# Optimization experiments

Hardware: AMD Instinct MI355X
Metric: run time of the kernel (lower is better)

Reference implementation:

```python
import jax
import jax.numpy as jnp
import numpy as np

NC = 80
TOPK = 10
STRIDES = (8, 16, 32)
GRIDS = ((80, 80), (40, 40), (20, 20))
ALPHA = 1.0
BETA = 6.0
EPS = 1e-9
B = 32
G = 20


def _pairwise_iou(b1, b2):
    # b1: [A,4], b2: [G,4] in x1y1x2y2 -> [A,G]
    lt = jnp.maximum(b1[:, None, :2], b2[None, :, :2])
    rb = jnp.minimum(b1[:, None, 2:], b2[None, :, 2:])
    wh = jnp.clip(rb - lt, 0.0)
    inter = wh[..., 0] * wh[..., 1]
    a1 = (b1[:, 2] - b1[:, 0]) * (b1[:, 3] - b1[:, 1])
    a2 = (b2[:, 2] - b2[:, 0]) * (b2[:, 3] - b2[:, 1])
    return inter / (a1[:, None] + a2[None, :] - inter + EPS)


def _assign_one(scores, reg, anchors, labels, boxes, stride):
    # Task-aligned assignment for one image at one FPN level.
    # scores: [A,NC] softmax probs, reg: [A,4] ltrb in stride units,
    # anchors: [A,2] grid centers, labels: [G] int, boxes: [G,4] pixels.
    A = scores.shape[0]
    g = labels.shape[0]
    anc_pix = anchors * stride                                    # [A,2]
    pd_boxes = jnp.concatenate(
        [anc_pix - reg[:, :2] * stride, anc_pix + reg[:, 2:] * stride], axis=-1
    )                                                             # [A,4]
    iou = _pairwise_iou(pd_boxes, boxes)                          # [A,G]
    cls_score = scores[:, labels]                                 # [A,G]
    align = (cls_score ** ALPHA) * (iou ** BETA)                  # [A,G]
    # candidate anchors: center strictly inside gt box
    lt_ok = (anc_pix[:, None, :] - boxes[None, :, :2]) > EPS
    rb_ok = (boxes[None, :, 2:] - anc_pix[:, None, :]) > EPS
    in_gts = jnp.all(jnp.concatenate([lt_ok, rb_ok], axis=-1), axis=-1)  # [A,G]
    metric = jnp.where(in_gts, align, 0.0)
    # top-k anchors per gt by alignment metric
    vals, idx = jax.lax.top_k(metric.T, TOPK)                     # [G,K]
    topk_mask = jnp.zeros((g, A), bool).at[jnp.arange(g)[:, None], idx].set(vals > EPS)
    is_pos = topk_mask.T & in_gts                                 # [A,G]
    # resolve anchors assigned to multiple gts by max IoU
    n_assign = is_pos.sum(axis=-1)
    best_gt = jnp.argmax(jnp.where(is_pos, iou, -1.0), axis=-1)   # [A]
    best_oh = jax.nn.one_hot(best_gt, g, dtype=bool)
    is_pos = jnp.where((n_assign > 1)[:, None], best_oh & is_pos, is_pos)
    fg_mask = is_pos.any(axis=-1)                                 # [A]
    assigned = jnp.argmax(is_pos, axis=-1)                        # [A]
    target_labels = jnp.where(fg_mask, labels[assigned], 0)
    return target_labels, fg_mask


def _level_loss(cls, reg, anc, gt_labels, gt_boxes, stride):
    # cls: [B,A,NC] logits, reg: [B,A,4], anc: [A,2]
    scores = jax.nn.softmax(jax.lax.stop_gradient(cls), axis=-1)
    tl, fg = jax.vmap(
        lambda s, r, l, b: _assign_one(s, r, anc, l, b, stride)
    )(scores, jax.lax.stop_gradient(reg), gt_labels, gt_boxes)
    logp = jax.nn.log_softmax(cls, axis=-1)
    ce = -jnp.take_along_axis(logp, tl[..., None], axis=-1)[..., 0]  # [B,A]
    return (ce * fg.astype(cls.dtype)).sum(), fg.sum()


def setup_inputs() -> dict:
    key = jax.random.key(0)
    ks = jax.random.split(key, 10)
    inp = {}
    for i, (h, w) in enumerate(GRIDS):
        inp[f"pred_cls_{i}"] = jax.random.normal(ks[i], (B, h * w, NC), jnp.float32)
        inp[f"pred_reg_{i}"] = jax.random.uniform(ks[3 + i], (B, h * w, 4), jnp.float32) * 4.0
    ancs = []
    for (h, w) in GRIDS:
        yy, xx = jnp.meshgrid(
            jnp.arange(h, dtype=jnp.float32) + 0.5,
            jnp.arange(w, dtype=jnp.float32) + 0.5,
            indexing="ij",
        )
        ancs.append(jnp.stack([xx.ravel(), yy.ravel()], axis=-1))
    inp["anchor_points"] = jnp.concatenate(ancs, axis=0)  # [8400,2] grid units
    cxcy = jax.random.uniform(ks[6], (B, G, 2), jnp.float32) * 600.0 + 20.0
    wh = jax.random.uniform(ks[7], (B, G, 2), jnp.float32) * 120.0 + 16.0
    boxes = jnp.concatenate([cxcy - wh / 2, cxcy + wh / 2], axis=-1)
    inp["gt_boxes"] = jnp.clip(boxes, 0.0, 640.0)
    inp["gt_labels"] = jax.random.randint(ks[8], (B, G), 0, NC)
    return inp


def reference(pred_cls_0, pred_cls_1, pred_cls_2,
              pred_reg_0, pred_reg_1, pred_reg_2,
              anchor_points, gt_boxes, gt_labels):
    pred_cls = [pred_cls_0, pred_cls_1, pred_cls_2]
    pred_reg = [pred_reg_0, pred_reg_1, pred_reg_2]
    sizes = [c.shape[1] for c in pred_cls]
    offs = np.cumsum([0] + sizes)
    total = jnp.zeros((), jnp.float32)
    n_pos = jnp.zeros((), jnp.int32)
    for i in range(3):
        anc = anchor_points[offs[i]:offs[i + 1]]
        l, k = _level_loss(pred_cls[i], pred_reg[i], anc, gt_labels, gt_boxes, STRIDES[i])
        total = total + l
        n_pos = n_pos + k.astype(jnp.int32)
    loss = total / jnp.maximum(n_pos, 1).astype(jnp.float32)
    return loss, n_pos
```

## Files before the change

### kernel.cpp

```cpp
#include <hip/hip_runtime.h>
#include <cstdint>
#include <cstddef>

#define NCLS 80
#define KTOP 10
#define NG   20
#define NB   32
#define A0   6400
#define A1   1600
#define A2   400
#define ATOT 8400
#define EPSF 1e-9f

#define NTHR   (NB * ATOT)
#define NBLK   ((NTHR + 255) / 256)
#define RECTCAP 512

__global__ __launch_bounds__(256) void phase1_logz(
    const float* __restrict__ cls0, const float* __restrict__ cls1,
    const float* __restrict__ cls2,
    const float* __restrict__ anchors, const float* __restrict__ gtb,
    float* __restrict__ logZ, uint32_t* __restrict__ mask)
{
    int t = blockIdx.x * 256 + threadIdx.x;
    if (t >= NTHR) return;
    mask[t] = 0;
    int b = t / ATOT, a = t % ATOT;

    const float* cls; int A; float stride;
    if (a < A0)           { cls = cls0; A = A0; stride = 8.f;  }
    else if (a < A0 + A1) { cls = cls1; A = A1; stride = 16.f; }
    else                  { cls = cls2; A = A2; stride = 32.f; }
    int al = (a < A0) ? a : (a < A0 + A1 ? a - A0 : a - A0 - A1);

    float ax = anchors[2 * a]     * stride;
    float ay = anchors[2 * a + 1] * stride;

    const float4* gb4 = reinterpret_cast<const float4*>(gtb + (size_t)b * NG * 4);
    bool any = false;
    #pragma unroll
    for (int g = 0; g < NG; ++g) {
        float4 gv = gb4[g];
        any = any || ((ax - gv.x > EPSF) && (ay - gv.y > EPSF) &&
                      (gv.z - ax > EPSF) && (gv.w - ay > EPSF));
    }
    if (!any) return;

    const float4* crow4 = reinterpret_cast<const float4*>(cls + ((size_t)b * A + al) * NCLS);
    float r[NCLS];
    float m = -1e30f;
    #pragma unroll
    for (int j = 0; j < NCLS / 4; ++j) {
        float4 v = crow4[j];
        r[4*j+0] = v.x; r[4*j+1] = v.y; r[4*j+2] = v.z; r[4*j+3] = v.w;
        m = fmaxf(m, fmaxf(fmaxf(v.x, v.y), fmaxf(v.z, v.w)));
    }
    float s = 0.f;
    #pragma unroll
    for (int c = 0; c < NCLS; ++c) s += __expf(r[c] - m);
    logZ[(size_t)b * ATOT + a] = m + __logf(s);
}

__global__ __launch_bounds__(64) void phase2_topk(
    const float* __restrict__ cls0, const float* __restrict__ reg0,
    const float* __restrict__ cls1, const float* __restrict__ reg1,
    const float* __restrict__ cls2, const float* __restrict__ reg2,
    const float* __restrict__ gtb, const int* __restrict__ gtl,
    const float* __restrict__ logZ, uint32_t* __restrict__ mask)
{
    int id  = blockIdx.x;
    int lvl = id % 3;
    int bg  = id / 3;
    int b = bg / NG, g = bg % NG;
    int lane = threadIdx.x;

    const float* cls; const float* reg; int off, A, W; float stride;
    if (lvl == 0)      { cls = cls0; reg = reg0; off = 0;     A = A0; W = 80; stride = 8.f;  }
    else if (lvl == 1) { cls = cls1; reg = reg1; off = A0;    A = A1; W = 40; stride = 16.f; }
    else               { cls = cls2; reg = reg2; off = A0+A1; A = A2; W = 20; stride = 32.f; }

    float4 gv = reinterpret_cast<const float4*>(gtb + (size_t)b * NG * 4)[g];
    int lbl = gtl[b * NG + g];

    float inv = 1.f / stride;
    int ix0 = max(0,     (int)floorf(gv.x * inv - 0.5f));
    int ix1 = min(W - 1, (int)ceilf (gv.z * inv - 0.5f));
    int iy0 = max(0,     (int)floorf(gv.y * inv - 0.5f));
    int iy1 = min(W - 1, (int)ceilf (gv.w * inv - 0.5f));
    int nx = ix1 - ix0 + 1, ny = iy1 - iy0 + 1;
    if (nx <= 0 || ny <= 0) return;
    int n = nx * ny; if (n > RECTCAP) n = RECTCAP;

    float area2 = (gv.z - gv.x) * (gv.w - gv.y);

    __shared__ unsigned long long key[RECTCAP];
    for (int i = lane; i < n; i += 64) {
        int iy = i / nx, ix = i - iy * nx;
        int gx = ix0 + ix, gy = iy0 + iy;
        float ax = ((float)gx + 0.5f) * stride;
        float ay = ((float)gy + 0.5f) * stride;
        unsigned long long kk = 0;
        bool ing = (ax - gv.x > EPSF) && (ay - gv.y > EPSF) &&
                   (gv.z - ax > EPSF) && (gv.w - ay > EPSF);
        if (ing) {
            int al = gy * W + gx;
            int a  = off + al;
            float4 rr = *reinterpret_cast<const float4*>(reg + ((size_t)b * A + al) * 4);
            float px1 = ax - rr.x * stride, py1 = ay - rr.y * stride;
            float px2 = ax + rr.z * stride, py2 = ay + rr.w * stride;
            float area1 = (px2 - px1) * (py2 - py1);
            float ltx = fmaxf(px1, gv.x), lty = fmaxf(py1, gv.y);
            float rbx = fminf(px2, gv.z), rby = fminf(py2, gv.w);
            float w = fmaxf(rbx - ltx, 0.f), h = fmaxf(rby - lty, 0.f);
            float inter = w * h;
            float iou = inter / (area1 + area2 - inter + EPSF);
            float lz = logZ[(size_t)b * ATOT + a];
            float c  = cls[((size_t)b * A + al) * NCLS + lbl];
            float sc = __expf(c - lz);
            float i2 = iou * iou;
            float met = sc * (i2 * i2 * i2);
            if (met > EPSF)
                kk = ((unsigned long long)__float_as_uint(met) << 32)
                   | (uint32_t)(ATOT - a);
        }
        key[i] = kk;
    }
    __syncthreads();

    for (int k = 0; k < KTOP; ++k) {
        unsigned long long bk = 0; int bs = -1;
        for (int i = lane; i < n; i += 64) {
            unsigned long long kk = key[i];
            if (kk > bk) { bk = kk; bs = i; }
        }
        #pragma unroll
        for (int sft = 32; sft > 0; sft >>= 1) {
            unsigned long long ok = __shfl_down(bk, sft);
            int os = __shfl_down(bs, sft);
            if (ok > bk) { bk = ok; bs = os; }
        }
        bk = __shfl(bk, 0); bs = __shfl(bs, 0);
        if (bk == 0) break;
        if (lane == 0) {
            int aa = ATOT - (int)(bk & 0xffffffffu);
            atomicOr(&mask[(size_t)b * ATOT + aa], 1u << g);
            key[bs] = 0;
        }
        __syncthreads();
    }
}

__global__ __launch_bounds__(256) void phase3_loss(
    const float* __restrict__ cls0, const float* __restrict__ reg0,
    const float* __restrict__ cls1, const float* __restrict__ reg1,
    const float* __restrict__ cls2, const float* __restrict__ reg2,
    const float* __restrict__ anchors, const float* __restrict__ gtb,
    const int* __restrict__ gtl,
    const uint32_t* __restrict__ mask, const float* __restrict__ logZ,
    float2* __restrict__ partials)
{
    int t = blockIdx.x * 256 + threadIdx.x;
    float ce = 0.f; float pc = 0.f;

    if (t < NTHR) {
        int b = t / ATOT, a = t % ATOT;
        uint32_t mk = mask[(size_t)b * ATOT + a];
        if (mk) {
            const float* cls; const float* reg; int off, A; float stride;
            if (a < A0)           { cls = cls0; reg = reg0; off = 0;     A = A0; stride = 8.f;  }
            else if (a < A0 + A1) { cls = cls1; reg = reg1; off = A0;    A = A1; stride = 16.f; }
            else                  { cls = cls2; reg = reg2; off = A0+A1; A = A2; stride = 32.f; }
            int al = a - off;

            float ax = anchors[2 * a]     * stride;
            float ay = anchors[2 * a + 1] * stride;
            float4 rr = *reinterpret_cast<const float4*>(reg + ((size_t)b * A + al) * 4);
            float px1 = ax - rr.x * stride, py1 = ay - rr.y * stride;
            float px2 = ax + rr.z * stride, py2 = ay + rr.w * stride;
            float area1 = (px2 - px1) * (py2 - py1);

            const float4* gb4 = reinterpret_cast<const float4*>(gtb + (size_t)b * NG * 4);

            float bestI = -1.f; int bestG = 0;
            uint32_t mm = mk;
            while (mm) {
                int g = __ffs(mm) - 1; mm &= mm - 1;
                float4 gv = gb4[g];
                float ltx = fmaxf(px1, gv.x), lty = fmaxf(py1, gv.y);
                float rbx = fminf(px2, gv.z), rby = fminf(py2, gv.w);
                float w = fmaxf(rbx - ltx, 0.f), h = fmaxf(rby - lty, 0.f);
                float inter = w * h;
                float area2 = (gv.z - gv.x) * (gv.w - gv.y);
                float iou = inter / (area1 + area2 - inter + EPSF);
                if (iou > bestI) { bestI = iou; bestG = g; }
            }
            int tl = gtl[b * NG + bestG];
            const float* crow = cls + ((size_t)b * A + al) * NCLS;
            ce = logZ[(size_t)b * ATOT + a] - crow[tl];
            pc = 1.f;
        }
    }

    #pragma unroll
    for (int sft = 32; sft > 0; sft >>= 1) {
        ce += __shfl_down(ce, sft);
        pc += __shfl_down(pc, sft);
    }
    __shared__ float sce[4];
    __shared__ float spc[4];
    int wid = threadIdx.x >> 6, lane = threadIdx.x & 63;
    if (lane == 0) { sce[wid] = ce; spc[wid] = pc; }
    __syncthreads();
    if (threadIdx.x == 0) {
        float2 p;
        p.x = sce[0] + sce[1] + sce[2] + sce[3];
        p.y = spc[0] + spc[1] + spc[2] + spc[3];
        partials[blockIdx.x] = p;
    }
}

__global__ __launch_bounds__(256) void finalize_loss(
    const float2* __restrict__ partials, float* __restrict__ out)
{
    float ce = 0.f, pc = 0.f;
    for (int i = threadIdx.x; i < NBLK; i += 256) {
        float2 p = partials[i];
        ce += p.x; pc += p.y;
    }
    #pragma unroll
    for (int sft = 32; sft > 0; sft >>= 1) {
        ce += __shfl_down(ce, sft);
        pc += __shfl_down(pc, sft);
    }
    __shared__ float sce[4];
    __shared__ float spc[4];
    int wid = threadIdx.x >> 6, lane = threadIdx.x & 63;
    if (lane == 0) { sce[wid] = ce; spc[wid] = pc; }
    __syncthreads();
    if (threadIdx.x == 0) {
        float total = sce[0] + sce[1] + sce[2] + sce[3];
        int   n     = (int)(spc[0] + spc[1] + spc[2] + spc[3]);
        float denom = (float)(n < 1 ? 1 : n);
        out[0] = total / denom;
        out[1] = (float)n;
    }
}

extern "C" void kernel_launch(void* const* d_in, const int* in_sizes, int n_in,
                              void* d_out, int out_size, void* d_ws, size_t ws_size,
                              hipStream_t stream)
{
    const float* cls0 = (const float*)d_in[0];
    const float* reg0 = (const float*)d_in[1];
    const float* cls1 = (const float*)d_in[2];
    const float* reg1 = (const float*)d_in[3];
    const float* cls2 = (const float*)d_in[4];
    const float* reg2 = (const float*)d_in[5];
    const float* anchors = (const float*)d_in[6];
    const float* gtb  = (const float*)d_in[7];
    const int*   gtl  = (const int*)d_in[8];

    float*    logZ     = (float*)d_ws;
    uint32_t* mask     = (uint32_t*)(logZ + (size_t)NB * ATOT);
    float2*   partials = (float2*)(mask + (size_t)NB * ATOT);

    phase1_logz<<<NBLK, 256, 0, stream>>>(cls0, cls1, cls2, anchors, gtb, logZ, mask);
    phase2_topk<<<NB * NG * 3, 64, 0, stream>>>(cls0, reg0, cls1, reg1, cls2, reg2,
                                                gtb, gtl, logZ, mask);
    phase3_loss<<<NBLK, 256, 0, stream>>>(cls0, reg0, cls1, reg1, cls2, reg2,
                                          anchors, gtb, gtl, mask, logZ, partials);
    finalize_loss<<<1, 256, 0, stream>>>(partials, (float*)d_out);
}
```

Before: 36.77 us.

## Replace dense anchor passes with sparse top-k winner lists and per-gt conflict resolution

Removes the dense per-anchor logZ pass and the dense mask/loss pass. Each (image, gt, level) block now computes log-softmax only for candidate anchors inside its gt rectangle, then writes its top-k winners with their IoU to a compact list. A second kernel resolves anchors claimed by several gts by scanning the winner lists of all gts at the same level, then computes cross-entropy only for the anchors it keeps. This cuts memory traffic and launches, but the logsumexp is now recomputed redundantly for anchors that fall inside several gt rectangles.

```diff
diff --git a/kernel.cpp b/kernel.cpp
--- a/kernel.cpp
+++ b/kernel.cpp
@@ -11,62 +11,14 @@
 #define A2   400
 #define ATOT 8400
 #define EPSF 1e-9f
-
-#define NTHR   (NB * ATOT)
-#define NBLK   ((NTHR + 255) / 256)
 #define RECTCAP 512
 
-__global__ __launch_bounds__(256) void phase1_logz(
-    const float* __restrict__ cls0, const float* __restrict__ cls1,
-    const float* __restrict__ cls2,
-    const float* __restrict__ anchors, const float* __restrict__ gtb,
-    float* __restrict__ logZ, uint32_t* __restrict__ mask)
-{
-    int t = blockIdx.x * 256 + threadIdx.x;
-    if (t >= NTHR) return;
-    mask[t] = 0;
-    int b = t / ATOT, a = t % ATOT;
-
-    const float* cls; int A; float stride;
-    if (a < A0)           { cls = cls0; A = A0; stride = 8.f;  }
-    else if (a < A0 + A1) { cls = cls1; A = A1; stride = 16.f; }
-    else                  { cls = cls2; A = A2; stride = 32.f; }
-    int al = (a < A0) ? a : (a < A0 + A1 ? a - A0 : a - A0 - A1);
-
-    float ax = anchors[2 * a]     * stride;
-    float ay = anchors[2 * a + 1] * stride;
-
-    const float4* gb4 = reinterpret_cast<const float4*>(gtb + (size_t)b * NG * 4);
-    bool any = false;
-    #pragma unroll
-    for (int g = 0; g < NG; ++g) {
-        float4 gv = gb4[g];
-        any = any || ((ax - gv.x > EPSF) && (ay - gv.y > EPSF) &&
-                      (gv.z - ax > EPSF) && (gv.w - ay > EPSF));
-    }
-    if (!any) return;
-
-    const float4* crow4 = reinterpret_cast<const float4*>(cls + ((size_t)b * A + al) * NCLS);
-    float r[NCLS];
-    float m = -1e30f;
-    #pragma unroll
-    for (int j = 0; j < NCLS / 4; ++j) {
-        float4 v = crow4[j];
-        r[4*j+0] = v.x; r[4*j+1] = v.y; r[4*j+2] = v.z; r[4*j+3] = v.w;
-        m = fmaxf(m, fmaxf(fmaxf(v.x, v.y), fmaxf(v.z, v.w)));
-    }
-    float s = 0.f;
-    #pragma unroll
-    for (int c = 0; c < NCLS; ++c) s += __expf(r[c] - m);
-    logZ[(size_t)b * ATOT + a] = m + __logf(s);
-}
-
-__global__ __launch_bounds__(64) void phase2_topk(
+__global__ __launch_bounds__(64) void k1_topk(
     const float* __restrict__ cls0, const float* __restrict__ reg0,
     const float* __restrict__ cls1, const float* __restrict__ reg1,
     const float* __restrict__ cls2, const float* __restrict__ reg2,
     const float* __restrict__ gtb, const int* __restrict__ gtl,
-    const float* __restrict__ logZ, uint32_t* __restrict__ mask)
+    int2* __restrict__ winners)
 {
     int id  = blockIdx.x;
     int lvl = id % 3;
@@ -88,18 +40,20 @@
     int iy0 = max(0,     (int)floorf(gv.y * inv - 0.5f));
     int iy1 = min(W - 1, (int)ceilf (gv.w * inv - 0.5f));
     int nx = ix1 - ix0 + 1, ny = iy1 - iy0 + 1;
-    if (nx <= 0 || ny <= 0) return;
-    int n = nx * ny; if (n > RECTCAP) n = RECTCAP;
+    int n = (nx > 0 && ny > 0) ? nx * ny : 0;
+    if (n > RECTCAP) n = RECTCAP;
 
     float area2 = (gv.z - gv.x) * (gv.w - gv.y);
 
     __shared__ unsigned long long key[RECTCAP];
+    __shared__ float iouA[RECTCAP];
+
     for (int i = lane; i < n; i += 64) {
         int iy = i / nx, ix = i - iy * nx;
         int gx = ix0 + ix, gy = iy0 + iy;
         float ax = ((float)gx + 0.5f) * stride;
         float ay = ((float)gy + 0.5f) * stride;
-        unsigned long long kk = 0;
+        unsigned long long kk = 0; float iou = 0.f;
         bool ing = (ax - gv.x > EPSF) && (ay - gv.y > EPSF) &&
                    (gv.z - ax > EPSF) && (gv.w - ay > EPSF);
         if (ing) {
@@ -113,17 +67,32 @@
             float rbx = fminf(px2, gv.z), rby = fminf(py2, gv.w);
             float w = fmaxf(rbx - ltx, 0.f), h = fmaxf(rby - lty, 0.f);
             float inter = w * h;
-            float iou = inter / (area1 + area2 - inter + EPSF);
-            float lz = logZ[(size_t)b * ATOT + a];
-            float c  = cls[((size_t)b * A + al) * NCLS + lbl];
-            float sc = __expf(c - lz);
+            iou = inter / (area1 + area2 - inter + EPSF);
+
+            const float4* crow4 =
+                reinterpret_cast<const float4*>(cls + ((size_t)b * A + al) * NCLS);
+            float r[NCLS];
+            float m = -1e30f;
+            #pragma unroll
+            for (int j = 0; j < NCLS / 4; ++j) {
+                float4 v = crow4[j];
+                r[4*j+0] = v.x; r[4*j+1] = v.y; r[4*j+2] = v.z; r[4*j+3] = v.w;
+                m = fmaxf(m, fmaxf(fmaxf(v.x, v.y), fmaxf(v.z, v.w)));
+            }
+            float s = 0.f;
+            #pragma unroll
+            for (int c = 0; c < NCLS; ++c) s += __expf(r[c] - m);
+            float lz = m + __logf(s);
+
+            float cl = cls[((size_t)b * A + al) * NCLS + lbl];
+            float sc = __expf(cl - lz);
             float i2 = iou * iou;
             float met = sc * (i2 * i2 * i2);
             if (met > EPSF)
                 kk = ((unsigned long long)__float_as_uint(met) << 32)
                    | (uint32_t)(ATOT - a);
         }
-        key[i] = kk;
+        key[i] = kk; iouA[i] = iou;
     }
     __syncthreads();
 
@@ -140,64 +109,76 @@
             if (ok > bk) { bk = ok; bs = os; }
         }
         bk = __shfl(bk, 0); bs = __shfl(bs, 0);
-        if (bk == 0) break;
+        if (bk == 0) {
+            if (lane >= k && lane < KTOP)
+                winners[(size_t)id * KTOP + lane] = make_int2(-1, 0);
+            break;
+        }
         if (lane == 0) {
             int aa = ATOT - (int)(bk & 0xffffffffu);
-            atomicOr(&mask[(size_t)b * ATOT + aa], 1u << g);
+            winners[(size_t)id * KTOP + k] = make_int2(aa, __float_as_int(iouA[bs]));
             key[bs] = 0;
         }
         __syncthreads();
     }
 }
 
-__global__ __launch_bounds__(256) void phase3_loss(
-    const float* __restrict__ cls0, const float* __restrict__ reg0,
-    const float* __restrict__ cls1, const float* __restrict__ reg1,
-    const float* __restrict__ cls2, const float* __restrict__ reg2,
-    const float* __restrict__ anchors, const float* __restrict__ gtb,
-    const int* __restrict__ gtl,
-    const uint32_t* __restrict__ mask, const float* __restrict__ logZ,
-    float2* __restrict__ partials)
-{
-    int t = blockIdx.x * 256 + threadIdx.x;
-    float ce = 0.f; float pc = 0.f;
-
-    if (t < NTHR) {
-        int b = t / ATOT, a = t % ATOT;
-        uint32_t mk = mask[(size_t)b * ATOT + a];
-        if (mk) {
-            const float* cls; const float* reg; int off, A; float stride;
-            if (a < A0)           { cls = cls0; reg = reg0; off = 0;     A = A0; stride = 8.f;  }
-            else if (a < A0 + A1) { cls = cls1; reg = reg1; off = A0;    A = A1; stride = 16.f; }
-            else                  { cls = cls2; reg = reg2; off = A0+A1; A = A2; stride = 32.f; }
-            int al = a - off;
-
-            float ax = anchors[2 * a]     * stride;
-            float ay = anchors[2 * a + 1] * stride;
-            float4 rr = *reinterpret_cast<const float4*>(reg + ((size_t)b * A + al) * 4);
-            float px1 = ax - rr.x * stride, py1 = ay - rr.y * stride;
-            float px2 = ax + rr.z * stride, py2 = ay + rr.w * stride;
-            float area1 = (px2 - px1) * (py2 - py1);
-
-            const float4* gb4 = reinterpret_cast<const float4*>(gtb + (size_t)b * NG * 4);
-
-            float bestI = -1.f; int bestG = 0;
-            uint32_t mm = mk;
-            while (mm) {
-                int g = __ffs(mm) - 1; mm &= mm - 1;
-                float4 gv = gb4[g];
-                float ltx = fmaxf(px1, gv.x), lty = fmaxf(py1, gv.y);
-                float rbx = fminf(px2, gv.z), rby = fminf(py2, gv.w);
-                float w = fmaxf(rbx - ltx, 0.f), h = fmaxf(rby - lty, 0.f);
-                float inter = w * h;
-                float area2 = (gv.z - gv.x) * (gv.w - gv.y);
-                float iou = inter / (area1 + area2 - inter + EPSF);
-                if (iou > bestI) { bestI = iou; bestG = g; }
+__global__ __launch_bounds__(64) void k2_resolve(
+    const float* __restrict__ cls0, const float* __restrict__ cls1,
+    const float* __restrict__ cls2, const int* __restrict__ gtl,
+    const int2* __restrict__ winners, float2* __restrict__ partials)
+{
+    int id = blockIdx.x;
+    int b = id / NG, g = id % NG;
+    int lane = threadIdx.x;
+
+    __shared__ int2 sh[NG * 3 * KTOP];
+    for (int i = lane; i < NG * 3 * KTOP; i += 64)
+        sh[i] = winners[(size_t)b * NG * 3 * KTOP + i];
+    __syncthreads();
+
+    float ce = 0.f, pc = 0.f;
+    if (lane < 3 * KTOP) {
+        int2 e = sh[g * 3 * KTOP + lane];
+        if (e.x >= 0) {
+            float eiou = __int_as_float(e.y);
+            int lvl_e = lane / KTOP;
+            bool beaten = false;
+            for (int gf = 0; gf < NG; ++gf) {
+                #pragma unroll
+                for (int s = 0; s < KTOP; ++s) {
+                    int2 f = sh[(gf * 3 + lvl_e) * KTOP + s];
+                    if (f.x == e.x) {
+                        float fiou = __int_as_float(f.y);
+                        if (fiou > eiou || (fiou == eiou && gf < g)) beaten = true;
+                    }
+                }
             }
-            int tl = gtl[b * NG + bestG];
-            const float* crow = cls + ((size_t)b * A + al) * NCLS;
-            ce = logZ[(size_t)b * ATOT + a] - crow[tl];
-            pc = 1.f;
+            if (!beaten) {
+                int a = e.x;
+                const float* cls; int A, off;
+                if (a < A0)           { cls = cls0; A = A0; off = 0;     }
+                else if (a < A0 + A1) { cls = cls1; A = A1; off = A0;    }
+                else                  { cls = cls2; A = A2; off = A0+A1; }
+                int al = a - off;
+                const float4* crow4 =
+                    reinterpret_cast<const float4*>(cls + ((size_t)b * A + al) * NCLS);
+                float r[NCLS];
+                float m = -1e30f;
+                #pragma unroll
+                for (int j = 0; j < NCLS / 4; ++j) {
+                    float4 v = crow4[j];
+                    r[4*j+0] = v.x; r[4*j+1] = v.y; r[4*j+2] = v.z; r[4*j+3] = v.w;
+                    m = fmaxf(m, fmaxf(fmaxf(v.x, v.y), fmaxf(v.z, v.w)));
+                }
+                float s2 = 0.f;
+                #pragma unroll
+                for (int c = 0; c < NCLS; ++c) s2 += __expf(r[c] - m);
+                float lz = m + __logf(s2);
+                int tl = gtl[b * NG + g];
+                ce = lz - cls[((size_t)b * A + al) * NCLS + tl];
+                pc = 1.f;
+            }
         }
     }
 
@@ -206,24 +187,14 @@
         ce += __shfl_down(ce, sft);
         pc += __shfl_down(pc, sft);
     }
-    __shared__ float sce[4];
-    __shared__ float spc[4];
-    int wid = threadIdx.x >> 6, lane = threadIdx.x & 63;
-    if (lane == 0) { sce[wid] = ce; spc[wid] = pc; }
-    __syncthreads();
-    if (threadIdx.x == 0) {
-        float2 p;
-        p.x = sce[0] + sce[1] + sce[2] + sce[3];
-        p.y = spc[0] + spc[1] + spc[2] + spc[3];
-        partials[blockIdx.x] = p;
-    }
-}
-
-__global__ __launch_bounds__(256) void finalize_loss(
+    if (lane == 0) partials[id] = make_float2(ce, pc);
+}
+
+__global__ __launch_bounds__(256) void k3_finalize(
     const float2* __restrict__ partials, float* __restrict__ out)
 {
     float ce = 0.f, pc = 0.f;
-    for (int i = threadIdx.x; i < NBLK; i += 256) {
+    for (int i = threadIdx.x; i < NB * NG; i += 256) {
         float2 p = partials[i];
         ce += p.x; pc += p.y;
     }
@@ -256,18 +227,14 @@
     const float* reg1 = (const float*)d_in[3];
     const float* cls2 = (const float*)d_in[4];
     const float* reg2 = (const float*)d_in[5];
-    const float* anchors = (const float*)d_in[6];
     const float* gtb  = (const float*)d_in[7];
     const int*   gtl  = (const int*)d_in[8];
 
-    float*    logZ     = (float*)d_ws;
-    uint32_t* mask     = (uint32_t*)(logZ + (size_t)NB * ATOT);
-    float2*   partials = (float2*)(mask + (size_t)NB * ATOT);
-
-    phase1_logz<<<NBLK, 256, 0, stream>>>(cls0, cls1, cls2, anchors, gtb, logZ, mask);
-    phase2_topk<<<NB * NG * 3, 64, 0, stream>>>(cls0, reg0, cls1, reg1, cls2, reg2,
-                                                gtb, gtl, logZ, mask);
-    phase3_loss<<<NBLK, 256, 0, stream>>>(cls0, reg0, cls1, reg1, cls2, reg2,
-                                          anchors, gtb, gtl, mask, logZ, partials);
-    finalize_loss<<<1, 256, 0, stream>>>(partials, (float*)d_out);
-}
+    int2*   winners  = (int2*)d_ws;
+    float2* partials = (float2*)(winners + NB * NG * 3 * KTOP);
+
+    k1_topk<<<NB * NG * 3, 64, 0, stream>>>(cls0, reg0, cls1, reg1, cls2, reg2,
+                                            gtb, gtl, winners);
+    k2_resolve<<<NB * NG, 64, 0, stream>>>(cls0, cls1, cls2, gtl, winners, partials);
+    k3_finalize<<<1, 256, 0, stream>>>(partials, (float*)d_out);
+}
```

Result: slower. 44.40 us (median of 3 runs) (+20.7%).

## Fuse top-k selection and conflict resolution into one per-image-level kernel

Applied to the files above, without the earlier changes.

Replaces the per-(image,gt,level) top-k kernel, the global mask array, and the full-grid loss pass with a single kernel per (image,level). Each wave handles five gts, keeps candidate keys in registers, and records winners with their IoU in shared memory. Anchors claimed by several gts are resolved by scanning that shared list, which removes the mask writes, the atomics and one full-size launch. The cost is fewer, heavier blocks (96) with serial per-wave work and a rectangle cap of 512 candidates per gt.

```diff
diff --git a/kernel.cpp b/kernel.cpp
--- a/kernel.cpp
+++ b/kernel.cpp
@@ -14,17 +14,16 @@
 
 #define NTHR   (NB * ATOT)
 #define NBLK   ((NTHR + 255) / 256)
-#define RECTCAP 512
-
-__global__ __launch_bounds__(256) void phase1_logz(
+#define KREG   8
+
+__global__ __launch_bounds__(256) void k1_logz(
     const float* __restrict__ cls0, const float* __restrict__ cls1,
     const float* __restrict__ cls2,
     const float* __restrict__ anchors, const float* __restrict__ gtb,
-    float* __restrict__ logZ, uint32_t* __restrict__ mask)
+    float* __restrict__ logZ)
 {
     int t = blockIdx.x * 256 + threadIdx.x;
     if (t >= NTHR) return;
-    mask[t] = 0;
     int b = t / ATOT, a = t % ATOT;
 
     const float* cls; int A; float stride;
@@ -61,143 +60,128 @@
     logZ[(size_t)b * ATOT + a] = m + __logf(s);
 }
 
-__global__ __launch_bounds__(64) void phase2_topk(
+__global__ __launch_bounds__(256) void k2_select_resolve(
     const float* __restrict__ cls0, const float* __restrict__ reg0,
     const float* __restrict__ cls1, const float* __restrict__ reg1,
     const float* __restrict__ cls2, const float* __restrict__ reg2,
     const float* __restrict__ gtb, const int* __restrict__ gtl,
-    const float* __restrict__ logZ, uint32_t* __restrict__ mask)
+    const float* __restrict__ logZ, float2* __restrict__ partials)
 {
     int id  = blockIdx.x;
     int lvl = id % 3;
-    int bg  = id / 3;
-    int b = bg / NG, g = bg % NG;
-    int lane = threadIdx.x;
+    int b   = id / 3;
+    int tid = threadIdx.x, wave = tid >> 6, lane = tid & 63;
 
     const float* cls; const float* reg; int off, A, W; float stride;
     if (lvl == 0)      { cls = cls0; reg = reg0; off = 0;     A = A0; W = 80; stride = 8.f;  }
     else if (lvl == 1) { cls = cls1; reg = reg1; off = A0;    A = A1; W = 40; stride = 16.f; }
     else               { cls = cls2; reg = reg2; off = A0+A1; A = A2; W = 20; stride = 32.f; }
 
-    float4 gv = reinterpret_cast<const float4*>(gtb + (size_t)b * NG * 4)[g];
-    int lbl = gtl[b * NG + g];
-
+    __shared__ int2 win[NG * KTOP];
+    for (int i = tid; i < NG * KTOP; i += 256) win[i] = make_int2(-1, 0);
+    __syncthreads();
+
+    const float4* gb4 = reinterpret_cast<const float4*>(gtb + (size_t)b * NG * 4);
     float inv = 1.f / stride;
-    int ix0 = max(0,     (int)floorf(gv.x * inv - 0.5f));
-    int ix1 = min(W - 1, (int)ceilf (gv.z * inv - 0.5f));
-    int iy0 = max(0,     (int)floorf(gv.y * inv - 0.5f));
-    int iy1 = min(W - 1, (int)ceilf (gv.w * inv - 0.5f));
-    int nx = ix1 - ix0 + 1, ny = iy1 - iy0 + 1;
-    if (nx <= 0 || ny <= 0) return;
-    int n = nx * ny; if (n > RECTCAP) n = RECTCAP;
-
-    float area2 = (gv.z - gv.x) * (gv.w - gv.y);
-
-    __shared__ unsigned long long key[RECTCAP];
-    for (int i = lane; i < n; i += 64) {
-        int iy = i / nx, ix = i - iy * nx;
-        int gx = ix0 + ix, gy = iy0 + iy;
-        float ax = ((float)gx + 0.5f) * stride;
-        float ay = ((float)gy + 0.5f) * stride;
-        unsigned long long kk = 0;
-        bool ing = (ax - gv.x > EPSF) && (ay - gv.y > EPSF) &&
-                   (gv.z - ax > EPSF) && (gv.w - ay > EPSF);
-        if (ing) {
-            int al = gy * W + gx;
-            int a  = off + al;
-            float4 rr = *reinterpret_cast<const float4*>(reg + ((size_t)b * A + al) * 4);
-            float px1 = ax - rr.x * stride, py1 = ay - rr.y * stride;
-            float px2 = ax + rr.z * stride, py2 = ay + rr.w * stride;
-            float area1 = (px2 - px1) * (py2 - py1);
-            float ltx = fmaxf(px1, gv.x), lty = fmaxf(py1, gv.y);
-            float rbx = fminf(px2, gv.z), rby = fminf(py2, gv.w);
-            float w = fmaxf(rbx - ltx, 0.f), h = fmaxf(rby - lty, 0.f);
-            float inter = w * h;
-            float iou = inter / (area1 + area2 - inter + EPSF);
-            float lz = logZ[(size_t)b * ATOT + a];
-            float c  = cls[((size_t)b * A + al) * NCLS + lbl];
-            float sc = __expf(c - lz);
-            float i2 = iou * iou;
-            float met = sc * (i2 * i2 * i2);
-            if (met > EPSF)
-                kk = ((unsigned long long)__float_as_uint(met) << 32)
-                   | (uint32_t)(ATOT - a);
+
+    for (int gg = 0; gg < 5; ++gg) {
+        int g = wave * 5 + gg;
+        float4 gv = gb4[g];
+        int lbl = gtl[b * NG + g];
+
+        int ix0 = max(0,     (int)floorf(gv.x * inv - 0.5f));
+        int ix1 = min(W - 1, (int)ceilf (gv.z * inv - 0.5f));
+        int iy0 = max(0,     (int)floorf(gv.y * inv - 0.5f));
+        int iy1 = min(W - 1, (int)ceilf (gv.w * inv - 0.5f));
+        int nx = ix1 - ix0 + 1, ny = iy1 - iy0 + 1;
+        int n = (nx > 0 && ny > 0) ? nx * ny : 0;
+        if (n > KREG * 64) n = KREG * 64;
+
+        float area2 = (gv.z - gv.x) * (gv.w - gv.y);
+
+        unsigned long long kreg[KREG]; float ioureg[KREG];
+        #pragma unroll
+        for (int j = 0; j < KREG; ++j) {
+            kreg[j] = 0; ioureg[j] = 0.f;
+            int i = j * 64 + lane;
+            if (i < n) {
+                int iy = i / nx, ix = i - iy * nx;
+                int gx = ix0 + ix, gy = iy0 + iy;
+                float ax = ((float)gx + 0.5f) * stride;
+                float ay = ((float)gy + 0.5f) * stride;
+                bool ing = (ax - gv.x > EPSF) && (ay - gv.y > EPSF) &&
+                           (gv.z - ax > EPSF) && (gv.w - ay > EPSF);
+                if (ing) {
+                    int al = gy * W + gx;
+                    int a  = off + al;
+                    float4 rr = *reinterpret_cast<const float4*>(reg + ((size_t)b * A + al) * 4);
+                    float px1 = ax - rr.x * stride, py1 = ay - rr.y * stride;
+                    float px2 = ax + rr.z * stride, py2 = ay + rr.w * stride;
+                    float area1 = (px2 - px1) * (py2 - py1);
+                    float ltx = fmaxf(px1, gv.x), lty = fmaxf(py1, gv.y);
+                    float rbx = fminf(px2, gv.z), rby = fminf(py2, gv.w);
+                    float w = fmaxf(rbx - ltx, 0.f), h = fmaxf(rby - lty, 0.f);
+                    float inter = w * h;
+                    float iou = inter / (area1 + area2 - inter + EPSF);
+                    float lz = logZ[(size_t)b * ATOT + a];
+                    float c  = cls[((size_t)b * A + al) * NCLS + lbl];
+                    float sc = __expf(c - lz);
+                    float i2 = iou * iou;
+                    float met = sc * (i2 * i2 * i2);
+                    if (met > EPSF) {
+                        kreg[j] = ((unsigned long long)__float_as_uint(met) << 32)
+                                | (uint32_t)(ATOT - a);
+                        ioureg[j] = iou;
+                    }
+                }
+            }
         }
-        key[i] = kk;
-    }
-    __syncthreads();
-
-    for (int k = 0; k < KTOP; ++k) {
-        unsigned long long bk = 0; int bs = -1;
-        for (int i = lane; i < n; i += 64) {
-            unsigned long long kk = key[i];
-            if (kk > bk) { bk = kk; bs = i; }
+
+        for (int k = 0; k < KTOP; ++k) {
+            unsigned long long bk = 0;
+            #pragma unroll
+            for (int j = 0; j < KREG; ++j) if (kreg[j] > bk) bk = kreg[j];
+            #pragma unroll
+            for (int sft = 32; sft > 0; sft >>= 1) {
+                unsigned long long ok = __shfl_down(bk, sft);
+                if (ok > bk) bk = ok;
+            }
+            bk = __shfl(bk, 0);
+            if (bk == 0) break;
+            #pragma unroll
+            for (int j = 0; j < KREG; ++j) {
+                if (kreg[j] == bk) {
+                    int aa = ATOT - (int)(bk & 0xffffffffu);
+                    win[g * KTOP + k] = make_int2(aa, __float_as_int(ioureg[j]));
+                    kreg[j] = 0;
+                }
+            }
         }
-        #pragma unroll
-        for (int sft = 32; sft > 0; sft >>= 1) {
-            unsigned long long ok = __shfl_down(bk, sft);
-            int os = __shfl_down(bs, sft);
-            if (ok > bk) { bk = ok; bs = os; }
-        }
-        bk = __shfl(bk, 0); bs = __shfl(bs, 0);
-        if (bk == 0) break;
-        if (lane == 0) {
-            int aa = ATOT - (int)(bk & 0xffffffffu);
-            atomicOr(&mask[(size_t)b * ATOT + aa], 1u << g);
-            key[bs] = 0;
-        }
-        __syncthreads();
-    }
-}
-
-__global__ __launch_bounds__(256) void phase3_loss(
-    const float* __restrict__ cls0, const float* __restrict__ reg0,
-    const float* __restrict__ cls1, const float* __restrict__ reg1,
-    const float* __restrict__ cls2, const float* __restrict__ reg2,
-    const float* __restrict__ anchors, const float* __restrict__ gtb,
-    const int* __restrict__ gtl,
-    const uint32_t* __restrict__ mask, const float* __restrict__ logZ,
-    float2* __restrict__ partials)
-{
-    int t = blockIdx.x * 256 + threadIdx.x;
-    float ce = 0.f; float pc = 0.f;
-
-    if (t < NTHR) {
-        int b = t / ATOT, a = t % ATOT;
-        uint32_t mk = mask[(size_t)b * ATOT + a];
-        if (mk) {
-            const float* cls; const float* reg; int off, A; float stride;
-            if (a < A0)           { cls = cls0; reg = reg0; off = 0;     A = A0; stride = 8.f;  }
-            else if (a < A0 + A1) { cls = cls1; reg = reg1; off = A0;    A = A1; stride = 16.f; }
-            else                  { cls = cls2; reg = reg2; off = A0+A1; A = A2; stride = 32.f; }
-            int al = a - off;
-
-            float ax = anchors[2 * a]     * stride;
-            float ay = anchors[2 * a + 1] * stride;
-            float4 rr = *reinterpret_cast<const float4*>(reg + ((size_t)b * A + al) * 4);
-            float px1 = ax - rr.x * stride, py1 = ay - rr.y * stride;
-            float px2 = ax + rr.z * stride, py2 = ay + rr.w * stride;
-            float area1 = (px2 - px1) * (py2 - py1);
-
-            const float4* gb4 = reinterpret_cast<const float4*>(gtb + (size_t)b * NG * 4);
-
-            float bestI = -1.f; int bestG = 0;
-            uint32_t mm = mk;
-            while (mm) {
-                int g = __ffs(mm) - 1; mm &= mm - 1;
-                float4 gv = gb4[g];
-                float ltx = fmaxf(px1, gv.x), lty = fmaxf(py1, gv.y);
-                float rbx = fminf(px2, gv.z), rby = fminf(py2, gv.w);
-                float w = fmaxf(rbx - ltx, 0.f), h = fmaxf(rby - lty, 0.f);
-                float inter = w * h;
-                float area2 = (gv.z - gv.x) * (gv.w - gv.y);
-                float iou = inter / (area1 + area2 - inter + EPSF);
-                if (iou > bestI) { bestI = iou; bestG = g; }
-            }
-            int tl = gtl[b * NG + bestG];
-            const float* crow = cls + ((size_t)b * A + al) * NCLS;
-            ce = logZ[(size_t)b * ATOT + a] - crow[tl];
-            pc = 1.f;
+    }
+    __syncthreads();
+
+    float ce = 0.f, pc = 0.f;
+    if (tid < NG * KTOP) {
+        int2 e = win[tid];
+        if (e.x >= 0) {
+            int g = tid / KTOP;
+            float eiou = __int_as_float(e.y);
+            bool beaten = false;
+            for (int i = 0; i < NG * KTOP; ++i) {
+                int2 f = win[i];
+                if (f.x == e.x) {
+                    float fiou = __int_as_float(f.y);
+                    int gf = i / KTOP;
+                    if (fiou > eiou || (fiou == eiou && gf < g)) beaten = true;
+                }
+            }
+            if (!beaten) {
+                int a = e.x, al = a - off;
+                float lz = logZ[(size_t)b * ATOT + a];
+                int tl = gtl[b * NG + g];
+                ce = lz - cls[((size_t)b * A + al) * NCLS + tl];
+                pc = 1.f;
+            }
         }
     }
 
@@ -208,38 +192,37 @@
     }
     __shared__ float sce[4];
     __shared__ float spc[4];
-    int wid = threadIdx.x >> 6, lane = threadIdx.x & 63;
-    if (lane == 0) { sce[wid] = ce; spc[wid] = pc; }
-    __syncthreads();
-    if (threadIdx.x == 0) {
+    if (lane == 0) { sce[wave] = ce; spc[wave] = pc; }
+    __syncthreads();
+    if (tid == 0) {
         float2 p;
         p.x = sce[0] + sce[1] + sce[2] + sce[3];
         p.y = spc[0] + spc[1] + spc[2] + spc[3];
-        partials[blockIdx.x] = p;
-    }
-}
-
-__global__ __launch_bounds__(256) void finalize_loss(
+        partials[id] = p;
+    }
+}
+
+__global__ __launch_bounds__(128) void k3_finalize(
     const float2* __restrict__ partials, float* __restrict__ out)
 {
     float ce = 0.f, pc = 0.f;
-    for (int i = threadIdx.x; i < NBLK; i += 256) {
-        float2 p = partials[i];
-        ce += p.x; pc += p.y;
+    if (threadIdx.x < NB * 3) {
+        float2 p = partials[threadIdx.x];
+        ce = p.x; pc = p.y;
     }
     #pragma unroll
     for (int sft = 32; sft > 0; sft >>= 1) {
         ce += __shfl_down(ce, sft);
         pc += __shfl_down(pc, sft);
     }
-    __shared__ float sce[4];
-    __shared__ float spc[4];
-    int wid = threadIdx.x >> 6, lane = threadIdx.x & 63;
-    if (lane == 0) { sce[wid] = ce; spc[wid] = pc; }
+    __shared__ float sce[2];
+    __shared__ float spc[2];
+    int wave = threadIdx.x >> 6, lane = threadIdx.x & 63;
+    if (lane == 0) { sce[wave] = ce; spc[wave] = pc; }
     __syncthreads();
     if (threadIdx.x == 0) {
-        float total = sce[0] + sce[1] + sce[2] + sce[3];
-        int   n     = (int)(spc[0] + spc[1] + spc[2] + spc[3]);
+        float total = sce[0] + sce[1];
+        int   n     = (int)(spc[0] + spc[1]);
         float denom = (float)(n < 1 ? 1 : n);
         out[0] = total / denom;
         out[1] = (float)n;
@@ -260,14 +243,12 @@
     const float* gtb  = (const float*)d_in[7];
     const int*   gtl  = (const int*)d_in[8];
 
-    float*    logZ     = (float*)d_ws;
-    uint32_t* mask     = (uint32_t*)(logZ + (size_t)NB * ATOT);
-    float2*   partials = (float2*)(mask + (size_t)NB * ATOT);
-
-    phase1_logz<<<NBLK, 256, 0, stream>>>(cls0, cls1, cls2, anchors, gtb, logZ, mask);
-    phase2_topk<<<NB * NG * 3, 64, 0, stream>>>(cls0, reg0, cls1, reg1, cls2, reg2,
-                                                gtb, gtl, logZ, mask);
-    phase3_loss<<<NBLK, 256, 0, stream>>>(cls0, reg0, cls1, reg1, cls2, reg2,
-                                          anchors, gtb, gtl, mask, logZ, partials);
-    finalize_loss<<<1, 256, 0, stream>>>(partials, (float*)d_out);
-}
+    float*  logZ     = (float*)d_ws;
+    float2* partials = (float2*)(logZ + (size_t)NB * ATOT);
+
+    k1_logz<<<NBLK, 256, 0, stream>>>(cls0, cls1, cls2, anchors, gtb, logZ);
+    k2_select_resolve<<<NB * 3, 256, 0, stream>>>(cls0, reg0, cls1, reg1,
+                                                  cls2, reg2, gtb, gtl,
+                                                  logZ, partials);
+    k3_finalize<<<1, 128, 0, stream>>>(partials, (float*)d_out);
+}
```

Result: slower. 76.34 us (+107.6%).
